# Kernel tuning notes

Hardware: AMD Instinct MI355X
Metric: run time of the kernel (lower is better)

## Reference

```python
import jax, jax.numpy as jnp
import numpy as np

N_HEADS = 16
N_KV_HEADS = 4
N_EMBD = 1024

def setup_inputs() -> dict:
    key = jax.random.key(0)
    kx, kq, kk, kv, ko = jax.random.split(key, 5)
    B, S, E = 2, 2048, N_EMBD
    head_dim = E // N_HEADS
    kv_dim = N_KV_HEADS * head_dim  # 256
    scale = 0.02
    return {
        "x": jax.random.normal(kx, (B, S, E), dtype=jnp.float32),
        "Wq": jax.random.normal(kq, (E, E), dtype=jnp.float32) * scale,
        "Wk": jax.random.normal(kk, (E, kv_dim), dtype=jnp.float32) * scale,
        "Wv": jax.random.normal(kv, (E, kv_dim), dtype=jnp.float32) * scale,
        "Wo": jax.random.normal(ko, (E, E), dtype=jnp.float32) * scale,
    }

def reference(x, Wq, Wk, Wv, Wo):
    B, S, E = x.shape
    H, KV = N_HEADS, N_KV_HEADS
    D = E // H            # head_dim = 64
    R = H // KV           # query heads per kv head = 4
    inv_sqrt_d = 1.0 / (D ** 0.5)

    q = (x @ Wq).reshape(B, S, KV, R, D)   # group query heads by kv group
    k = (x @ Wk).reshape(B, S, KV, D)
    v = (x @ Wv).reshape(B, S, KV, D)

    # repeat_interleave(kv, R, dim=heads) == broadcast kv head g to query heads (g, r)
    scores = jnp.einsum('bqgrd,bkgd->bgrqk', q, k) * inv_sqrt_d  # [B,KV,R,S,S]
    causal = jnp.tril(jnp.ones((S, S), dtype=bool))
    scores = jnp.where(causal, scores, jnp.float32(-jnp.inf))
    attn = jax.nn.softmax(scores, axis=-1)

    out = jnp.einsum('bgrqk,bkgd->bqgrd', attn, v).reshape(B, S, E)
    return out @ Wo
```

## Files before the change

kernel.cpp:

```cpp
#include <hip/hip_runtime.h>
#include <hip/hip_bf16.h>

#define B_SZ   2
#define S_LEN  2048
#define E_DIM  1024
#define H_Q    16
#define H_KV   4
#define HD     64
#define KV_DIM 256
#define M_ROWS (B_SZ * S_LEN)
#define N_QT   (S_LEN / 64)

typedef short bf16x4 __attribute__((ext_vector_type(4)));
typedef short bf16x8 __attribute__((ext_vector_type(8)));
typedef float f32x4  __attribute__((ext_vector_type(4)));
typedef unsigned u32x2 __attribute__((ext_vector_type(2)));

#define MFMA16x32(a, b, c) __builtin_amdgcn_mfma_f32_16x16x32_bf16(a, b, c, 0, 0, 0)

#if __has_builtin(__builtin_amdgcn_mfma_f32_16x16x16bf16_1k)
#define MFMA_PV(a, b, c) __builtin_amdgcn_mfma_f32_16x16x16bf16_1k(a, b, c, 0, 0, 0)
#elif __has_builtin(__builtin_amdgcn_mfma_f32_16x16x16_bf16)
#define MFMA_PV(a, b, c) __builtin_amdgcn_mfma_f32_16x16x16_bf16(a, b, c, 0, 0, 0)
#else
static __device__ inline f32x4 mfma_pv_asm(bf16x4 a, bf16x4 b, f32x4 c) {
    asm volatile("v_mfma_f32_16x16x16_bf16 %0, %1, %2, %0"
                 : "+v"(c) : "v"(a), "v"(b));
    return c;
}
#define MFMA_PV(a, b, c) mfma_pv_asm(a, b, c)
#endif

static __device__ __forceinline__ short f32_to_bf16(float f) {
    unsigned u = __builtin_bit_cast(unsigned, f);
    u += 0x7fffu + ((u >> 16) & 1u);
    return (short)(u >> 16);
}

static __device__ __forceinline__ unsigned pack2_trunc(float a, float b) {
    unsigned ua = __builtin_bit_cast(unsigned, a);
    unsigned ub = __builtin_bit_cast(unsigned, b);
    return (ua >> 16) | (ub & 0xffff0000u);
}

static __device__ __forceinline__ void load_lds16(const short* g, short* l) {
    __builtin_amdgcn_global_load_lds(
        (const __attribute__((address_space(1))) void*)g,
        (__attribute__((address_space(3))) void*)l, 16, 0, 0);
}

__global__ __launch_bounds__(256)
void cast_f32_bf16(const float* __restrict__ x, short* __restrict__ y, int n4) {
    int i = blockIdx.x * 256 + threadIdx.x;
    if (i < n4) {
        float4 v = ((const float4*)x)[i];
        bf16x4 o;
        o[0] = f32_to_bf16(v.x); o[1] = f32_to_bf16(v.y);
        o[2] = f32_to_bf16(v.z); o[3] = f32_to_bf16(v.w);
        ((bf16x4*)y)[i] = o;
    }
}

__global__ __launch_bounds__(256)
void transpose_cast(const float* __restrict__ W, short* __restrict__ Wt,
                    int K, int N) {
    __shared__ float t[32][33];
    const int n0 = blockIdx.x * 32, k0 = blockIdx.y * 32;
    const int tx = threadIdx.x, ty = threadIdx.y;
#pragma unroll
    for (int i = 0; i < 32; i += 8)
        t[ty + i][tx] = W[(long)(k0 + ty + i) * N + n0 + tx];
    __syncthreads();
#pragma unroll
    for (int i = 0; i < 32; i += 8)
        Wt[(long)(n0 + ty + i) * K + k0 + tx] = f32_to_bf16(t[tx][ty + i]);
}

__device__ __forceinline__ void gemm128(const short* __restrict__ Ab,
                                        const short* __restrict__ Btb,
                                        int K, short* As, short* Bs,
                                        f32x4 acc[4][4]) {
    const int tid  = threadIdx.x;
    const int wave = tid >> 6;
    const int lane = tid & 63;
    const int lq   = lane & 15;
    const int lg   = lane >> 4;
    const int wm   = wave >> 1;
    const int wn   = wave & 1;
    const int lrow = lane >> 2;
    const int lkc  = (lane & 3) * 8;

#pragma unroll
    for (int i = 0; i < 4; ++i)
#pragma unroll
        for (int j = 0; j < 4; ++j) acc[i][j] = (f32x4){0.f, 0.f, 0.f, 0.f};

    for (int k0 = 0; k0 < K; k0 += 32) {
        __syncthreads();
#pragma unroll
        for (int it = 0; it < 2; ++it) {
            const int m0 = wave * 32 + it * 16;
            const int m  = m0 + lrow;
            load_lds16(Ab  + (size_t)m * K + k0 + lkc, As + m0 * 32);
            load_lds16(Btb + (size_t)m * K + k0 + lkc, Bs + m0 * 32);
        }
        __syncthreads();
        bf16x8 af[4], bfr[4];
#pragma unroll
        for (int i = 0; i < 4; ++i) {
            af[i]  = *(const bf16x8*)&As[(wm * 64 + i * 16 + lq) * 32 + lg * 8];
            bfr[i] = *(const bf16x8*)&Bs[(wn * 64 + i * 16 + lq) * 32 + lg * 8];
        }
#pragma unroll
        for (int i = 0; i < 4; ++i)
#pragma unroll
            for (int j = 0; j < 4; ++j)
                acc[i][j] = MFMA16x32(af[i], bfr[j], acc[i][j]);
    }
}

__global__ __launch_bounds__(256)
void qkv_gemm(const short* __restrict__ xbf,
              const short* __restrict__ Wqt, const short* __restrict__ Wkt,
              const short* __restrict__ Wvt,
              short* __restrict__ Qbf, short* __restrict__ Kbf,
              short* __restrict__ Vbf, float qscale) {
    __shared__ short As[128 * 32];
    __shared__ short Bs[128 * 32];
    const int nb = blockIdx.x;
    const int mb = blockIdx.y;
    const short* Bt; short* out; int ldc, ncol0; float alpha;
    if (nb < 8) {
        Bt = Wqt + (size_t)nb * 128 * E_DIM;
        out = Qbf; ldc = E_DIM; ncol0 = nb * 128; alpha = qscale;
    } else if (nb < 10) {
        Bt = Wkt + (size_t)(nb - 8) * 128 * E_DIM;
        out = Kbf; ldc = KV_DIM; ncol0 = (nb - 8) * 128; alpha = 1.f;
    } else {
        Bt = Wvt + (size_t)(nb - 10) * 128 * E_DIM;
        out = Vbf; ldc = KV_DIM; ncol0 = (nb - 10) * 128; alpha = 1.f;
    }
    f32x4 acc[4][4];
    gemm128(xbf + (size_t)mb * 128 * E_DIM, Bt, E_DIM, As, Bs, acc);

    const int lane = threadIdx.x & 63, wave = threadIdx.x >> 6;
    const int lq = lane & 15, lg = lane >> 4, wm = wave >> 1, wn = wave & 1;
#pragma unroll
    for (int i = 0; i < 4; ++i)
#pragma unroll
        for (int r = 0; r < 4; ++r) {
            const size_t row = (size_t)mb * 128 + wm * 64 + i * 16 + lg * 4 + r;
#pragma unroll
            for (int j = 0; j < 4; ++j)
                out[row * ldc + ncol0 + wn * 64 + j * 16 + lq] =
                    f32_to_bf16(acc[i][j][r] * alpha);
        }
}

__global__ __launch_bounds__(256)
void gemm_o(const short* __restrict__ Abf, const short* __restrict__ Wot,
            float* __restrict__ C) {
    __shared__ short As[128 * 32];
    __shared__ short Bs[128 * 32];
    const int nb = blockIdx.x;
    const int mb = blockIdx.y;
    f32x4 acc[4][4];
    gemm128(Abf + (size_t)mb * 128 * E_DIM,
            Wot + (size_t)nb * 128 * E_DIM, E_DIM, As, Bs, acc);

    const int lane = threadIdx.x & 63, wave = threadIdx.x >> 6;
    const int lq = lane & 15, lg = lane >> 4, wm = wave >> 1, wn = wave & 1;
#pragma unroll
    for (int i = 0; i < 4; ++i)
#pragma unroll
        for (int r = 0; r < 4; ++r) {
            const size_t row = (size_t)mb * 128 + wm * 64 + i * 16 + lg * 4 + r;
#pragma unroll
            for (int j = 0; j < 4; ++j)
                C[row * E_DIM + nb * 128 + wn * 64 + j * 16 + lq] =
                    acc[i][j][r];
        }
}

struct KVregs { bf16x8 k[2], v[2]; };

__device__ __forceinline__ void stage_load(const short* __restrict__ Kb,
                                           const short* __restrict__ Vb,
                                           long rowbase, int g, KVregs& kv) {
    const int tid = threadIdx.x;
#pragma unroll
    for (int it = 0; it < 2; ++it) {
        const int c   = tid + it * 256;
        const int row = c >> 3;
        const int ch  = c & 7;
        const long src = (rowbase + row) * KV_DIM + g * HD + ch * 8;
        kv.k[it] = *(const bf16x8*)(Kb + src);
        kv.v[it] = *(const bf16x8*)(Vb + src);
    }
}

__device__ __forceinline__ void stage_write(short (*Ks)[72], short (*Vt)[68],
                                            const KVregs& kv) {
    const int tid = threadIdx.x;
#pragma unroll
    for (int it = 0; it < 2; ++it) {
        const int c   = tid + it * 256;
        const int row = c >> 3;
        const int ch  = c & 7;
        *(bf16x8*)&Ks[row][ch * 8] = kv.k[it];
#pragma unroll
        for (int i = 0; i < 8; ++i) Vt[ch * 8 + i][row] = kv.v[it][i];
    }
}

__global__ __launch_bounds__(256)
void flash_mfma(const short* __restrict__ Qb,
                const short* __restrict__ Kb,
                const short* __restrict__ Vb,
                short* __restrict__ Ob) {
    const int pair = blockIdx.x;
    const int h    = blockIdx.y;
    const int b    = blockIdx.z;
    const int g    = h >> 2;

    const int tid  = threadIdx.x;
    const int wave = tid >> 6;
    const int lane = tid & 63;
    const int lq   = lane & 15;
    const int lg   = lane >> 4;

    __shared__ short Ks[2][64][72];
    __shared__ short Vt[2][64][68];

    for (int rep = 0; rep < 2; ++rep) {
        const int qt = rep ? (N_QT - 1 - pair) : pair;
        const int qs = qt * 64;

        const short* qrow =
            Qb + ((long)(b * S_LEN + qs + wave * 16 + lq)) * E_DIM + h * HD;
        const bf16x8 qf0 = *(const bf16x8*)(qrow + lg * 8);
        const bf16x8 qf1 = *(const bf16x8*)(qrow + 32 + lg * 8);

        f32x4 o[4];
#pragma unroll
        for (int dc = 0; dc < 4; ++dc) o[dc] = (f32x4){0.f, 0.f, 0.f, 0.f};
        float m_run = -INFINITY, l_run = 0.f;

        KVregs kv;
        stage_load(Kb, Vb, (long)b * S_LEN, g, kv);
        stage_write(Ks[0], Vt[0], kv);
        __syncthreads();

        int p = 0;
        for (int kt = 0; kt <= qt; ++kt) {
            if (kt < qt)
                stage_load(Kb, Vb, (long)b * S_LEN + (kt + 1) * 64, g, kv);

            const int cmax = (kt == qt) ? wave : 3;
            f32x4 s[4];
#pragma unroll
            for (int c = 0; c < 4; ++c) {
                if (c > cmax) continue;
                bf16x8 kf0 = *(const bf16x8*)&Ks[p][c * 16 + lq][lg * 8];
                bf16x8 kf1 = *(const bf16x8*)&Ks[p][c * 16 + lq][32 + lg * 8];
                f32x4 acc = (f32x4){0.f, 0.f, 0.f, 0.f};
                acc = MFMA16x32(kf0, qf0, acc);
                acc = MFMA16x32(kf1, qf1, acc);
                s[c] = acc;
            }

            if (kt == qt) {
#pragma unroll
                for (int r = 0; r < 4; ++r)
                    if (lg * 4 + r > lq) s[wave][r] = -INFINITY;
            }

            float mt = -INFINITY;
#pragma unroll
            for (int c = 0; c < 4; ++c) {
                if (c > cmax) continue;
#pragma unroll
                for (int r = 0; r < 4; ++r) mt = fmaxf(mt, s[c][r]);
            }
            mt = fmaxf(mt, __shfl_xor(mt, 16));
            mt = fmaxf(mt, __shfl_xor(mt, 32));
            const float m_new = fmaxf(m_run, mt);
            const float alpha = exp2f(m_run - m_new);
            float psum = 0.f;
#pragma unroll
            for (int c = 0; c < 4; ++c) {
                if (c > cmax) continue;
#pragma unroll
                for (int r = 0; r < 4; ++r) {
                    float pe = exp2f(s[c][r] - m_new);
                    s[c][r] = pe;
                    psum += pe;
                }
            }
            psum += __shfl_xor(psum, 16);
            psum += __shfl_xor(psum, 32);
            l_run = l_run * alpha + psum;
            m_run = m_new;

#pragma unroll
            for (int r = 0; r < 4; ++r) {
                const float aT = __shfl(alpha, lg * 4 + r);
                o[0][r] *= aT; o[1][r] *= aT; o[2][r] *= aT; o[3][r] *= aT;
            }

#pragma unroll
            for (int c = 0; c < 4; ++c) {
                if (c > cmax) continue;
                u32x2 packed;
                packed[0] = pack2_trunc(s[c][0], s[c][1]);
                packed[1] = pack2_trunc(s[c][2], s[c][3]);
                bf16x4 pa = __builtin_bit_cast(bf16x4, packed);
#pragma unroll
                for (int dc = 0; dc < 4; ++dc) {
                    bf16x4 vf =
                        *(const bf16x4*)&Vt[p][dc * 16 + lq][c * 16 + lg * 4];
                    o[dc] = MFMA_PV(pa, vf, o[dc]);
                }
            }

            if (kt < qt) stage_write(Ks[p ^ 1], Vt[p ^ 1], kv);
            __syncthreads();
            p ^= 1;
        }

#pragma unroll
        for (int r = 0; r < 4; ++r) {
            const float lT  = __shfl(l_run, lg * 4 + r);
            const float inv = 1.f / lT;
            const long base =
                ((long)(b * S_LEN + qs + wave * 16 + lg * 4 + r)) * E_DIM +
                h * HD + lq;
#pragma unroll
            for (int dc = 0; dc < 4; ++dc)
                Ob[base + dc * 16] = f32_to_bf16(o[dc][r] * inv);
        }
    }
}

extern "C" void kernel_launch(void* const* d_in, const int* in_sizes, int n_in,
                              void* d_out, int out_size, void* d_ws, size_t ws_size,
                              hipStream_t stream) {
    const float* x  = (const float*)d_in[0];
    const float* Wq = (const float*)d_in[1];
    const float* Wk = (const float*)d_in[2];
    const float* Wv = (const float*)d_in[3];
    const float* Wo = (const float*)d_in[4];
    float* out = (float*)d_out;

    short* xbf = (short*)d_ws;
    short* Wqt = xbf + (size_t)M_ROWS * E_DIM;
    short* Wkt = Wqt + (size_t)E_DIM * E_DIM;
    short* Wvt = Wkt + (size_t)KV_DIM * E_DIM;
    short* Wot = Wvt + (size_t)KV_DIM * E_DIM;
    short* Qbf = Wot + (size_t)E_DIM * E_DIM;
    short* Kbf = Qbf + (size_t)M_ROWS * E_DIM;
    short* Vbf = Kbf + (size_t)M_ROWS * KV_DIM;
    short* Abf = Vbf + (size_t)M_ROWS * KV_DIM;

    const float qscale = 0.125f * 1.44269504088896340736f;

    cast_f32_bf16<<<dim3(M_ROWS * E_DIM / 4 / 256), dim3(256), 0, stream>>>(
        x, xbf, M_ROWS * E_DIM / 4);
    transpose_cast<<<dim3(E_DIM / 32, E_DIM / 32), dim3(32, 8), 0, stream>>>(
        Wq, Wqt, E_DIM, E_DIM);
    transpose_cast<<<dim3(KV_DIM / 32, E_DIM / 32), dim3(32, 8), 0, stream>>>(
        Wk, Wkt, E_DIM, KV_DIM);
    transpose_cast<<<dim3(KV_DIM / 32, E_DIM / 32), dim3(32, 8), 0, stream>>>(
        Wv, Wvt, E_DIM, KV_DIM);
    transpose_cast<<<dim3(E_DIM / 32, E_DIM / 32), dim3(32, 8), 0, stream>>>(
        Wo, Wot, E_DIM, E_DIM);

    qkv_gemm<<<dim3(12, M_ROWS / 128), dim3(256), 0, stream>>>(
        xbf, Wqt, Wkt, Wvt, Qbf, Kbf, Vbf, qscale);
    flash_mfma<<<dim3(N_QT / 2, H_Q, B_SZ), dim3(256), 0, stream>>>(
        Qbf, Kbf, Vbf, Abf);
    gemm_o<<<dim3(E_DIM / 128, M_ROWS / 128), dim3(256), 0, stream>>>(
        Abf, Wot, out);
}
```

Baseline: 205.3 us.

## Fuse prep kernels, shrink GEMM M-tile to 64, swizzle V transpose in LDS

Merges the x cast and four weight transpose-cast launches into one prep kernel, cutting launch overhead. Halves the GEMM M-tile to 64 rows, which doubles the block count for the QKV and output projections and fills more of the CUs, at the cost of less reuse per block. Replaces the padded V-transpose LDS array with an XOR-style rotated column layout meant to avoid bank conflicts without padding.

New measurement: 198.2 us. 1.04x faster.

```diff
diff --git a/kernel.cpp b/kernel.cpp
--- a/kernel.cpp
+++ b/kernel.cpp
@@ -49,37 +49,55 @@
         (__attribute__((address_space(3))) void*)l, 16, 0, 0);
 }
 
+__device__ __forceinline__ void transpose_body(const float* __restrict__ W,
+                                               short* __restrict__ Wt,
+                                               int K, int N, int bx, int by) {
+    __shared__ float t[32][33];
+    const int n0 = bx * 32, k0 = by * 32;
+    const int tx = threadIdx.x & 31, ty = threadIdx.x >> 5;
+#pragma unroll
+    for (int i = 0; i < 32; i += 8)
+        t[ty + i][tx] = W[(long)(k0 + ty + i) * N + n0 + tx];
+    __syncthreads();
+#pragma unroll
+    for (int i = 0; i < 32; i += 8)
+        Wt[(long)(n0 + ty + i) * K + k0 + tx] = f32_to_bf16(t[tx][ty + i]);
+}
+
 __global__ __launch_bounds__(256)
-void cast_f32_bf16(const float* __restrict__ x, short* __restrict__ y, int n4) {
-    int i = blockIdx.x * 256 + threadIdx.x;
-    if (i < n4) {
+void prep(const float* __restrict__ x,
+          const float* __restrict__ Wq, const float* __restrict__ Wk,
+          const float* __restrict__ Wv, const float* __restrict__ Wo,
+          short* __restrict__ xbf, short* __restrict__ Wqt,
+          short* __restrict__ Wkt, short* __restrict__ Wvt,
+          short* __restrict__ Wot) {
+    const int bid = blockIdx.x;
+    if (bid < 4096) {
+        const int i = bid * 256 + threadIdx.x;
         float4 v = ((const float4*)x)[i];
         bf16x4 o;
         o[0] = f32_to_bf16(v.x); o[1] = f32_to_bf16(v.y);
         o[2] = f32_to_bf16(v.z); o[3] = f32_to_bf16(v.w);
-        ((bf16x4*)y)[i] = o;
-    }
-}
-
-__global__ __launch_bounds__(256)
-void transpose_cast(const float* __restrict__ W, short* __restrict__ Wt,
-                    int K, int N) {
-    __shared__ float t[32][33];
-    const int n0 = blockIdx.x * 32, k0 = blockIdx.y * 32;
-    const int tx = threadIdx.x, ty = threadIdx.y;
-#pragma unroll
-    for (int i = 0; i < 32; i += 8)
-        t[ty + i][tx] = W[(long)(k0 + ty + i) * N + n0 + tx];
-    __syncthreads();
-#pragma unroll
-    for (int i = 0; i < 32; i += 8)
-        Wt[(long)(n0 + ty + i) * K + k0 + tx] = f32_to_bf16(t[tx][ty + i]);
-}
-
-__device__ __forceinline__ void gemm128(const short* __restrict__ Ab,
-                                        const short* __restrict__ Btb,
-                                        int K, short* As, short* Bs,
-                                        f32x4 acc[4][4]) {
+        ((bf16x4*)xbf)[i] = o;
+    } else if (bid < 5120) {
+        const int r = bid - 4096;
+        transpose_body(Wq, Wqt, E_DIM, E_DIM, r & 31, r >> 5);
+    } else if (bid < 5376) {
+        const int r = bid - 5120;
+        transpose_body(Wk, Wkt, E_DIM, KV_DIM, r & 7, r >> 3);
+    } else if (bid < 5632) {
+        const int r = bid - 5376;
+        transpose_body(Wv, Wvt, E_DIM, KV_DIM, r & 7, r >> 3);
+    } else {
+        const int r = bid - 5632;
+        transpose_body(Wo, Wot, E_DIM, E_DIM, r & 31, r >> 5);
+    }
+}
+
+__device__ __forceinline__ void gemm64x128(const short* __restrict__ Ab,
+                                           const short* __restrict__ Btb,
+                                           int K, short* As, short* Bs,
+                                           f32x4 acc[2][4]) {
     const int tid  = threadIdx.x;
     const int wave = tid >> 6;
     const int lane = tid & 63;
@@ -91,28 +109,31 @@
     const int lkc  = (lane & 3) * 8;
 
 #pragma unroll
-    for (int i = 0; i < 4; ++i)
+    for (int i = 0; i < 2; ++i)
 #pragma unroll
         for (int j = 0; j < 4; ++j) acc[i][j] = (f32x4){0.f, 0.f, 0.f, 0.f};
 
     for (int k0 = 0; k0 < K; k0 += 32) {
         __syncthreads();
+        {
+            const int m0 = wave * 16;
+            load_lds16(Ab + (size_t)(m0 + lrow) * K + k0 + lkc, As + m0 * 32);
+        }
 #pragma unroll
         for (int it = 0; it < 2; ++it) {
             const int m0 = wave * 32 + it * 16;
-            const int m  = m0 + lrow;
-            load_lds16(Ab  + (size_t)m * K + k0 + lkc, As + m0 * 32);
-            load_lds16(Btb + (size_t)m * K + k0 + lkc, Bs + m0 * 32);
+            load_lds16(Btb + (size_t)(m0 + lrow) * K + k0 + lkc, Bs + m0 * 32);
         }
         __syncthreads();
-        bf16x8 af[4], bfr[4];
-#pragma unroll
-        for (int i = 0; i < 4; ++i) {
-            af[i]  = *(const bf16x8*)&As[(wm * 64 + i * 16 + lq) * 32 + lg * 8];
-            bfr[i] = *(const bf16x8*)&Bs[(wn * 64 + i * 16 + lq) * 32 + lg * 8];
-        }
-#pragma unroll
-        for (int i = 0; i < 4; ++i)
+        bf16x8 af[2], bfr[4];
+#pragma unroll
+        for (int i = 0; i < 2; ++i)
+            af[i] = *(const bf16x8*)&As[(wm * 32 + i * 16 + lq) * 32 + lg * 8];
+#pragma unroll
+        for (int j = 0; j < 4; ++j)
+            bfr[j] = *(const bf16x8*)&Bs[(wn * 64 + j * 16 + lq) * 32 + lg * 8];
+#pragma unroll
+        for (int i = 0; i < 2; ++i)
 #pragma unroll
             for (int j = 0; j < 4; ++j)
                 acc[i][j] = MFMA16x32(af[i], bfr[j], acc[i][j]);
@@ -125,7 +146,7 @@
               const short* __restrict__ Wvt,
               short* __restrict__ Qbf, short* __restrict__ Kbf,
               short* __restrict__ Vbf, float qscale) {
-    __shared__ short As[128 * 32];
+    __shared__ short As[64 * 32];
     __shared__ short Bs[128 * 32];
     const int nb = blockIdx.x;
     const int mb = blockIdx.y;
@@ -140,16 +161,16 @@
         Bt = Wvt + (size_t)(nb - 10) * 128 * E_DIM;
         out = Vbf; ldc = KV_DIM; ncol0 = (nb - 10) * 128; alpha = 1.f;
     }
-    f32x4 acc[4][4];
-    gemm128(xbf + (size_t)mb * 128 * E_DIM, Bt, E_DIM, As, Bs, acc);
+    f32x4 acc[2][4];
+    gemm64x128(xbf + (size_t)mb * 64 * E_DIM, Bt, E_DIM, As, Bs, acc);
 
     const int lane = threadIdx.x & 63, wave = threadIdx.x >> 6;
     const int lq = lane & 15, lg = lane >> 4, wm = wave >> 1, wn = wave & 1;
 #pragma unroll
-    for (int i = 0; i < 4; ++i)
+    for (int i = 0; i < 2; ++i)
 #pragma unroll
         for (int r = 0; r < 4; ++r) {
-            const size_t row = (size_t)mb * 128 + wm * 64 + i * 16 + lg * 4 + r;
+            const size_t row = (size_t)mb * 64 + wm * 32 + i * 16 + lg * 4 + r;
 #pragma unroll
             for (int j = 0; j < 4; ++j)
                 out[row * ldc + ncol0 + wn * 64 + j * 16 + lq] =
@@ -160,21 +181,21 @@
 __global__ __launch_bounds__(256)
 void gemm_o(const short* __restrict__ Abf, const short* __restrict__ Wot,
             float* __restrict__ C) {
-    __shared__ short As[128 * 32];
+    __shared__ short As[64 * 32];
     __shared__ short Bs[128 * 32];
     const int nb = blockIdx.x;
     const int mb = blockIdx.y;
-    f32x4 acc[4][4];
-    gemm128(Abf + (size_t)mb * 128 * E_DIM,
-            Wot + (size_t)nb * 128 * E_DIM, E_DIM, As, Bs, acc);
+    f32x4 acc[2][4];
+    gemm64x128(Abf + (size_t)mb * 64 * E_DIM,
+               Wot + (size_t)nb * 128 * E_DIM, E_DIM, As, Bs, acc);
 
     const int lane = threadIdx.x & 63, wave = threadIdx.x >> 6;
     const int lq = lane & 15, lg = lane >> 4, wm = wave >> 1, wn = wave & 1;
 #pragma unroll
-    for (int i = 0; i < 4; ++i)
+    for (int i = 0; i < 2; ++i)
 #pragma unroll
         for (int r = 0; r < 4; ++r) {
-            const size_t row = (size_t)mb * 128 + wm * 64 + i * 16 + lg * 4 + r;
+            const size_t row = (size_t)mb * 64 + wm * 32 + i * 16 + lg * 4 + r;
 #pragma unroll
             for (int j = 0; j < 4; ++j)
                 C[row * E_DIM + nb * 128 + wn * 64 + j * 16 + lq] =
@@ -199,7 +220,7 @@
     }
 }
 
-__device__ __forceinline__ void stage_write(short (*Ks)[72], short (*Vt)[68],
+__device__ __forceinline__ void stage_write(short (*Ks)[72], short (*Vt)[64],
                                             const KVregs& kv) {
     const int tid = threadIdx.x;
 #pragma unroll
@@ -208,8 +229,9 @@
         const int row = c >> 3;
         const int ch  = c & 7;
         *(bf16x8*)&Ks[row][ch * 8] = kv.k[it];
-#pragma unroll
-        for (int i = 0; i < 8; ++i) Vt[ch * 8 + i][row] = kv.v[it][i];
+        const int col = (row + 8 * ch) & 63;
+#pragma unroll
+        for (int i = 0; i < 8; ++i) Vt[ch * 8 + i][col] = kv.v[it][i];
     }
 }
 
@@ -230,7 +252,7 @@
     const int lg   = lane >> 4;
 
     __shared__ short Ks[2][64][72];
-    __shared__ short Vt[2][64][68];
+    __shared__ short Vt[2][64][64];
 
     for (int rep = 0; rep < 2; ++rep) {
         const int qt = rep ? (N_QT - 1 - pair) : pair;
@@ -317,8 +339,9 @@
                 bf16x4 pa = __builtin_bit_cast(bf16x4, packed);
 #pragma unroll
                 for (int dc = 0; dc < 4; ++dc) {
-                    bf16x4 vf =
-                        *(const bf16x4*)&Vt[p][dc * 16 + lq][c * 16 + lg * 4];
+                    const int d    = dc * 16 + lq;
+                    const int col0 = (c * 16 + lg * 4 + 8 * (d >> 3)) & 63;
+                    bf16x4 vf = *(const bf16x4*)&Vt[p][d][col0];
                     o[dc] = MFMA_PV(pa, vf, o[dc]);
                 }
             }
@@ -364,21 +387,12 @@
 
     const float qscale = 0.125f * 1.44269504088896340736f;
 
-    cast_f32_bf16<<<dim3(M_ROWS * E_DIM / 4 / 256), dim3(256), 0, stream>>>(
-        x, xbf, M_ROWS * E_DIM / 4);
-    transpose_cast<<<dim3(E_DIM / 32, E_DIM / 32), dim3(32, 8), 0, stream>>>(
-        Wq, Wqt, E_DIM, E_DIM);
-    transpose_cast<<<dim3(KV_DIM / 32, E_DIM / 32), dim3(32, 8), 0, stream>>>(
-        Wk, Wkt, E_DIM, KV_DIM);
-    transpose_cast<<<dim3(KV_DIM / 32, E_DIM / 32), dim3(32, 8), 0, stream>>>(
-        Wv, Wvt, E_DIM, KV_DIM);
-    transpose_cast<<<dim3(E_DIM / 32, E_DIM / 32), dim3(32, 8), 0, stream>>>(
-        Wo, Wot, E_DIM, E_DIM);
-
-    qkv_gemm<<<dim3(12, M_ROWS / 128), dim3(256), 0, stream>>>(
+    prep<<<dim3(6656), dim3(256), 0, stream>>>(
+        x, Wq, Wk, Wv, Wo, xbf, Wqt, Wkt, Wvt, Wot);
+    qkv_gemm<<<dim3(12, M_ROWS / 64), dim3(256), 0, stream>>>(
         xbf, Wqt, Wkt, Wvt, Qbf, Kbf, Vbf, qscale);
     flash_mfma<<<dim3(N_QT / 2, H_Q, B_SZ), dim3(256), 0, stream>>>(
         Qbf, Kbf, Vbf, Abf);
-    gemm_o<<<dim3(E_DIM / 128, M_ROWS / 128), dim3(256), 0, stream>>>(
+    gemm_o<<<dim3(E_DIM / 128, M_ROWS / 64), dim3(256), 0, stream>>>(
         Abf, Wot, out);
 }
```
